# Performance work log

Measured on AMD Instinct MI355X. Metric: run time of the kernel, lower is better.

## Reference

```python
import jax, jax.numpy as jnp
import numpy as np

H = 8  # num_heads
NEG = -1e6  # mask fill value used by the torch masked_softmax


def layernorm(x, g, b, eps=1e-5):
    mu = jnp.mean(x, axis=-1, keepdims=True)
    var = jnp.mean(jnp.square(x - mu), axis=-1, keepdims=True)
    return (x - mu) * jax.lax.rsqrt(var + eps) * g + b


def setup_inputs() -> dict:
    key = jax.random.key(0)
    ks = jax.random.split(key, 10)
    B, S, D, F = 8, 1024, 512, 2048
    s = 0.02
    return {
        "X": jax.random.normal(ks[0], (B, S, D), jnp.float32),
        "valid_lens": jax.random.randint(ks[1], (B,), 1, S + 1, jnp.int32),
        "ln1_g": jnp.ones((D,), jnp.float32),
        "ln1_b": jnp.zeros((D,), jnp.float32),
        "Wq": jax.random.normal(ks[2], (D, D), jnp.float32) * s,
        "Wk": jax.random.normal(ks[3], (D, D), jnp.float32) * s,
        "Wv": jax.random.normal(ks[4], (D, D), jnp.float32) * s,
        "Wo": jax.random.normal(ks[5], (D, D), jnp.float32) * s,
        "ln2_g": jnp.ones((D,), jnp.float32),
        "ln2_b": jnp.zeros((D,), jnp.float32),
        "W1": jax.random.normal(ks[6], (D, F), jnp.float32) * s,
        "b1": jnp.zeros((F,), jnp.float32),
        "W2": jax.random.normal(ks[7], (F, D), jnp.float32) * s,
        "b2": jnp.zeros((D,), jnp.float32),
    }


def vit_block(X, valid_lens, ln1_g, ln1_b, Wq, Wk, Wv, Wo, ln2_g, ln2_b, W1, b1, W2, b2):
    B, S, D = X.shape
    dh = D // H
    h = layernorm(X, ln1_g, ln1_b)
    # project and split heads: [B, S, H, dh]
    q = (h @ Wq).reshape(B, S, H, dh)
    k = (h @ Wk).reshape(B, S, H, dh)
    v = (h @ Wv).reshape(B, S, H, dh)
    scores = jnp.einsum("bqhd,bkhd->bhqk", q, k) / jnp.sqrt(jnp.float32(dh))
    # mask keys >= valid_len[b] with -1e6 (as in masked_softmax)
    mask = jnp.arange(S)[None, None, None, :] < valid_lens[:, None, None, None]
    scores = jnp.where(mask, scores, NEG)
    attn = jax.nn.softmax(scores, axis=-1)
    out = jnp.einsum("bhqk,bkhd->bqhd", attn, v).reshape(B, S, D)
    X = X + out @ Wo
    h2 = layernorm(X, ln2_g, ln2_b)
    mlp = jax.nn.gelu(h2 @ W1 + b1, approximate=False) @ W2 + b2
    return X + mlp


def reference(X, valid_lens, ln1_g, ln1_b, Wq, Wk, Wv, Wo, ln2_g, ln2_b, W1, b1, W2, b2):
    return vit_block(X, valid_lens, ln1_g, ln1_b, Wq, Wk, Wv, Wo, ln2_g, ln2_b, W1, b1, W2, b2)
```

## Files before the change

### kernel.cpp

```cpp
#include <hip/hip_runtime.h>
#include <math.h>

#define BB 8
#define SS 1024
#define DD 512
#define FF 2048
#define NH 8
#define MM (BB * SS)
#define LDQKV 1536

using bf8 = __attribute__((ext_vector_type(8))) short;
using f4  = __attribute__((ext_vector_type(4))) float;

#define AS1 __attribute__((address_space(1)))
#define AS3 __attribute__((address_space(3)))

__device__ __forceinline__ void gload16(const void* g, void* l) {
  __builtin_amdgcn_global_load_lds((AS1 const void*)g, (AS3 void*)l, 16, 0, 0);
}

template <int N> __device__ __forceinline__ void wait_vm() {
  if constexpr (N == 0)      asm volatile("s_waitcnt vmcnt(0)" ::: "memory");
  else if constexpr (N == 3) asm volatile("s_waitcnt vmcnt(3)" ::: "memory");
  else if constexpr (N == 4) asm volatile("s_waitcnt vmcnt(4)" ::: "memory");
  else if constexpr (N == 8) asm volatile("s_waitcnt vmcnt(8)" ::: "memory");
  else                       asm volatile("s_waitcnt vmcnt(16)" ::: "memory");
  __builtin_amdgcn_sched_barrier(0);
}

__device__ __forceinline__ void bar() {
  __builtin_amdgcn_sched_barrier(0);
  __builtin_amdgcn_s_barrier();
  __builtin_amdgcn_sched_barrier(0);
}

__device__ __forceinline__ void lgk0() {
  asm volatile("s_waitcnt lgkmcnt(0)" ::: "memory");
  __builtin_amdgcn_sched_barrier(0);
}

__device__ __forceinline__ unsigned short f2b(float f) {
  union { float f; unsigned u; } v; v.f = f;
  unsigned r = v.u + 0x7fffu + ((v.u >> 16) & 1u);
  return (unsigned short)(r >> 16);
}

__device__ __forceinline__ float gelu_f(float x) {
  float ax = fabsf(x) * 0.70710678118654752f;
  float t = 1.0f / (1.0f + 0.3275911f * ax);
  float poly = t * (0.254829592f +
               t * (-0.284496736f +
               t * (1.421413741f +
               t * (-1.453152027f + t * 1.061405429f))));
  float erfv = 1.0f - poly * __expf(-ax * ax);
  erfv = copysignf(erfv, x);
  return 0.5f * x * (1.0f + erfv);
}

__global__ __launch_bounds__(256) void ln_bf16(const float* __restrict__ x,
                                               const float* __restrict__ g,
                                               const float* __restrict__ bta,
                                               unsigned short* __restrict__ out) {
  int wave = threadIdx.x >> 6, lane = threadIdx.x & 63;
  int row = (blockIdx.x << 2) + wave;
  const float* xr = x + (size_t)row * DD;
  int base = lane << 3;
  float4 v0 = *(const float4*)(xr + base);
  float4 v1 = *(const float4*)(xr + base + 4);
  float s  = v0.x + v0.y + v0.z + v0.w + v1.x + v1.y + v1.z + v1.w;
  float sq = v0.x*v0.x + v0.y*v0.y + v0.z*v0.z + v0.w*v0.w
           + v1.x*v1.x + v1.y*v1.y + v1.z*v1.z + v1.w*v1.w;
  for (int m = 32; m; m >>= 1) { s += __shfl_xor(s, m); sq += __shfl_xor(sq, m); }
  float mu  = s * (1.0f / DD);
  float var = sq * (1.0f / DD) - mu * mu;
  float rs  = rsqrtf(var + 1e-5f);
  float xv[8], go[8], bo[8];
  *(float4*)(xv) = v0; *(float4*)(xv + 4) = v1;
  *(float4*)(go)     = *(const float4*)(g + base);
  *(float4*)(go + 4) = *(const float4*)(g + base + 4);
  *(float4*)(bo)     = *(const float4*)(bta + base);
  *(float4*)(bo + 4) = *(const float4*)(bta + base + 4);
  union { unsigned short u[8]; uint4 v; } ov;
#pragma unroll
  for (int i = 0; i < 8; i++) ov.u[i] = f2b((xv[i] - mu) * rs * go[i] + bo[i]);
  *(uint4*)(out + (size_t)row * DD + base) = ov.v;
}

__global__ __launch_bounds__(256) void tconv(const float* __restrict__ in,
                                             unsigned short* __restrict__ outp,
                                             int K, int N) {
  __shared__ float tile[32][33];
  int n0 = blockIdx.x << 5, k0 = blockIdx.y << 5;
  int c = threadIdx.x & 31, r = threadIdx.x >> 5;
#pragma unroll
  for (int i = 0; i < 4; i++)
    tile[r + 8 * i][c] = in[(size_t)(k0 + r + 8 * i) * N + n0 + c];
  __syncthreads();
#pragma unroll
  for (int i = 0; i < 4; i++)
    outp[(size_t)(n0 + r + 8 * i) * K + k0 + c] = f2b(tile[c][r + 8 * i]);
}

__global__ __launch_bounds__(256) void tconv4(
    const float* __restrict__ s0, const float* __restrict__ s1,
    const float* __restrict__ s2, const float* __restrict__ s3,
    unsigned short* __restrict__ d0, unsigned short* __restrict__ d1,
    unsigned short* __restrict__ d2, unsigned short* __restrict__ d3) {
  __shared__ float tile[32][33];
  const float* in; unsigned short* outp;
  switch (blockIdx.z) {
    case 0: in = s0; outp = d0; break;
    case 1: in = s1; outp = d1; break;
    case 2: in = s2; outp = d2; break;
    default: in = s3; outp = d3; break;
  }
  int n0 = blockIdx.x << 5, k0 = blockIdx.y << 5;
  int c = threadIdx.x & 31, r = threadIdx.x >> 5;
#pragma unroll
  for (int i = 0; i < 4; i++)
    tile[r + 8 * i][c] = in[(size_t)(k0 + r + 8 * i) * DD + n0 + c];
  __syncthreads();
#pragma unroll
  for (int i = 0; i < 4; i++)
    outp[(size_t)(n0 + r + 8 * i) * DD + k0 + c] = f2b(tile[c][r + 8 * i]);
}

template <int ACT>
__global__ __launch_bounds__(128, 2) void gemm_wp(
    const unsigned short* __restrict__ A,
    const unsigned short* __restrict__ Bt,
    const float* __restrict__ bias,
    unsigned short* __restrict__ Cb,
    int M, int N, int K, int gxn) {
  __shared__ unsigned short Lds[2][2][4096];
  int tid = threadIdx.x, wv = tid >> 6, lane = tid & 63;

  int bid = blockIdx.x, cpx = (int)gridDim.x >> 3;
  int swz = (bid & 7) * cpx + (bid >> 3);
  int tile = swz * 2 + wv;
  int m0 = (tile / gxn) << 6, n0 = (tile % gxn) << 6;

  int r4 = lane & 15, ksl = lane >> 4;
  int srow = lane >> 2;
  int gs = (lane & 3) ^ ((lane >> 3) & 3);

  const unsigned short* aSrc = A + (size_t)(m0 + srow) * K + gs * 8;
  const unsigned short* bSrc = Bt + (size_t)(n0 + srow) * K + gs * 8;
  char* lw = (char*)&Lds[wv][0][0];

  f4 acc[4][4];
#pragma unroll
  for (int i = 0; i < 4; i++)
#pragma unroll
    for (int j = 0; j < 4; j++) acc[i][j] = (f4){0.f, 0.f, 0.f, 0.f};

  auto STAGE = [&](int buf, int t) {
    int k0 = t << 5;
#pragma unroll
    for (int ch = 0; ch < 4; ch++) {
      gload16(aSrc + (size_t)(ch * 16) * K + k0, &Lds[wv][buf][ch * 512]);
      gload16(bSrc + (size_t)(ch * 16) * K + k0, &Lds[wv][buf][2048 + ch * 512]);
    }
  };

  auto COMPUTE = [&](int buf) {
    char* ab = lw + buf * 8192;
    bf8 af[4], bfr[4];
#pragma unroll
    for (int mi = 0; mi < 4; mi++) {
      int r = mi * 16 + r4;
      af[mi] = *(const bf8*)(ab + r * 64 + ((ksl ^ ((r >> 1) & 3)) << 4));
    }
#pragma unroll
    for (int ni = 0; ni < 4; ni++) {
      int r = ni * 16 + r4;
      bfr[ni] = *(const bf8*)(ab + 4096 + r * 64 + ((ksl ^ ((r >> 1) & 3)) << 4));
    }
    __builtin_amdgcn_s_setprio(1);
#pragma unroll
    for (int mi = 0; mi < 4; mi++)
#pragma unroll
      for (int ni = 0; ni < 4; ni++)
        acc[mi][ni] = __builtin_amdgcn_mfma_f32_16x16x32_bf16(
            af[mi], bfr[ni], acc[mi][ni], 0, 0, 0);
    __builtin_amdgcn_s_setprio(0);
  };

  int nt = K >> 5;
  STAGE(0, 0);
  STAGE(1, 1);
  for (int t = 0; t < nt; t++) {
    if (t + 1 < nt) wait_vm<8>();
    else            wait_vm<0>();
    COMPUTE(t & 1);
    if (t + 2 < nt) {
      lgk0();
      STAGE(t & 1, t + 2);
    }
  }

  int rq = ksl << 2;
  float bv[4];
#pragma unroll
  for (int ni = 0; ni < 4; ni++)
    bv[ni] = bias ? bias[n0 + ni * 16 + r4] : 0.0f;
#pragma unroll
  for (int ni = 0; ni < 4; ni++) {
    int col = n0 + ni * 16 + r4;
#pragma unroll
    for (int mi = 0; mi < 4; mi++) {
#pragma unroll
      for (int j = 0; j < 4; j++) {
        int row = m0 + mi * 16 + rq + j;
        float v = acc[mi][ni][j] + bv[ni];
        if (ACT) v = gelu_f(v);
        Cb[(size_t)row * N + col] = f2b(v);
      }
    }
  }
}

template <int BM, int BN, int ACT, int MINW>
__global__ __launch_bounds__(256, MINW) void gemm_t(
    const unsigned short* __restrict__ A,
    const unsigned short* __restrict__ Bt,
    const float* __restrict__ bias,
    const float* __restrict__ res,
    float* __restrict__ Cf,
    unsigned short* __restrict__ Cb,
    int M, int N, int K, int gx) {
  constexpr int WM = BM / 2, WN = BN / 2;
  constexpr int FM = WM / 16, FN = WN / 16;
  constexpr int NCHA = BM / 16;
  constexpr int NCH = (BM + BN) / 16;
  constexpr int L = NCH / 4;
  __shared__ unsigned short As[2][BM * 32];
  __shared__ unsigned short Bs[2][BN * 32];
  int tid = threadIdx.x, wid = tid >> 6, lane = tid & 63;

  int bid = blockIdx.x, cpx = (int)gridDim.x >> 3;
  int swz = (bid & 7) * cpx + (bid >> 3);
  int m0 = (swz / gx) * BM, n0 = (swz % gx) * BN;

  int wm = (wid >> 1) * WM, wn = (wid & 1) * WN;
  int r4 = lane & 15, ksl = lane >> 4;
  int srow = lane >> 2, gs = (lane & 3) ^ ((lane >> 3) & 3);

  f4 acc[FM][FN];
#pragma unroll
  for (int i = 0; i < FM; i++)
#pragma unroll
    for (int j = 0; j < FN; j++) acc[i][j] = (f4){0.f, 0.f, 0.f, 0.f};

  auto STAGE = [&](int buf, int t) {
    int k0 = t << 5;
#pragma unroll
    for (int i = 0; i < L; i++) {
      int c = wid * L + i;
      if (c < NCHA)
        gload16(A + (size_t)(m0 + c * 16 + srow) * K + k0 + gs * 8,
                &As[buf][c * 512]);
      else
        gload16(Bt + (size_t)(n0 + (c - NCHA) * 16 + srow) * K + k0 + gs * 8,
                &Bs[buf][(c - NCHA) * 512]);
    }
  };

  auto COMPUTE = [&](int buf) {
    bf8 af[FM], bfr[FN];
#pragma unroll
    for (int mi = 0; mi < FM; mi++) {
      int r = wm + mi * 16 + r4;
      af[mi] = *(const bf8*)((const char*)&As[buf][0] + r * 64 +
                             ((ksl ^ ((r >> 1) & 3)) << 4));
    }
#pragma unroll
    for (int ni = 0; ni < FN; ni++) {
      int r = wn + ni * 16 + r4;
      bfr[ni] = *(const bf8*)((const char*)&Bs[buf][0] + r * 64 +
                              ((ksl ^ ((r >> 1) & 3)) << 4));
    }
    __builtin_amdgcn_s_setprio(1);
#pragma unroll
    for (int mi = 0; mi < FM; mi++)
#pragma unroll
      for (int ni = 0; ni < FN; ni++)
        acc[mi][ni] = __builtin_amdgcn_mfma_f32_16x16x32_bf16(
            af[mi], bfr[ni], acc[mi][ni], 0, 0, 0);
    __builtin_amdgcn_s_setprio(0);
  };

  int nt = K >> 5;
  STAGE(0, 0);
  STAGE(1, 1);
  for (int t = 0; t < nt; t++) {
    if (t + 1 < nt) wait_vm<L>();
    else            wait_vm<0>();
    bar();
    COMPUTE(t & 1);
    bar();
    if (t + 2 < nt) STAGE(t & 1, t + 2);
  }

  int rq = ksl << 2;
  float bv[FN];
#pragma unroll
  for (int ni = 0; ni < FN; ni++)
    bv[ni] = bias ? bias[n0 + wn + ni * 16 + r4] : 0.0f;
#pragma unroll
  for (int ni = 0; ni < FN; ni++) {
    int col = n0 + wn + ni * 16 + r4;
#pragma unroll
    for (int mi = 0; mi < FM; mi++) {
#pragma unroll
      for (int j = 0; j < 4; j++) {
        int row = m0 + wm + mi * 16 + rq + j;
        float v = acc[mi][ni][j] + bv[ni];
        if (ACT) v = gelu_f(v);
        if (res) v += res[(size_t)row * N + col];
        if (Cf) Cf[(size_t)row * N + col] = v;
        else    Cb[(size_t)row * N + col] = f2b(v);
      }
    }
  }
}

__global__ __launch_bounds__(256) void attn_mfma(
    const unsigned short* __restrict__ QKV,
    const int* __restrict__ vlen,
    unsigned short* __restrict__ AO) {
  __shared__ unsigned short Qs[64 * 64];
  __shared__ unsigned short Ks[64 * 64];
  __shared__ unsigned short Vt[64 * 64];
  __shared__ unsigned short Ps[64 * 64];
  int b = blockIdx.z, h = blockIdx.y, q0 = blockIdx.x << 6;
  int tid = threadIdx.x, wid = tid >> 6, lane = tid & 63;
  int vl = vlen[b];
  int r4 = lane & 15, ksl = lane >> 4;

  int srow = lane >> 3;
  int gs = (lane & 7) ^ srow;
  {
    const unsigned short* qsrc =
        QKV + (size_t)(b * SS + q0 + wid * 16 + srow) * LDQKV + h * 64 + gs * 8;
    gload16(qsrc, Qs + wid * 1024);
    gload16(qsrc + (size_t)8 * LDQKV, Qs + wid * 1024 + 512);
  }
  const unsigned short* kbase =
      QKV + (size_t)(b * SS + wid * 16 + srow) * LDQKV + DD + h * 64 + gs * 8;
  int vp = tid & 31, vdg = (tid >> 5) << 3;
  const unsigned short* vbase =
      QKV + (size_t)(b * SS + 2 * vp) * LDQKV + 2 * DD + h * 64 + vdg;

  f4 o[4];
#pragma unroll
  for (int i = 0; i < 4; i++) o[i] = (f4){0.f, 0.f, 0.f, 0.f};
  float mrun[4], lrun[4];
#pragma unroll
  for (int j = 0; j < 4; j++) { mrun[j] = -3e38f; lrun[j] = 0.0f; }

  int ntiles = (vl + 63) >> 6;
  if (ntiles > 16) ntiles = 16;

  for (int t = 0; t < ntiles; t++) {
    int kg0 = t << 6;
    const unsigned short* ks = kbase + (size_t)kg0 * LDQKV;
    gload16(ks, Ks + wid * 1024);
    gload16(ks + (size_t)8 * LDQKV, Ks + wid * 1024 + 512);
    {
      const unsigned short* v0 = vbase + (size_t)kg0 * LDQKV;
      const unsigned short* v1 = v0 + LDQKV;
      unsigned short va[8], vb[8];
      *(uint4*)va = *(const uint4*)v0;
      *(uint4*)vb = *(const uint4*)v1;
#pragma unroll
      for (int i = 0; i < 8; i++) {
        int d = vdg + i;
        unsigned val = (unsigned)va[i] | ((unsigned)vb[i] << 16);
        int byte = (d << 7) + (((vp >> 2) ^ (d & 7)) << 4) + ((vp & 3) << 2);
        *(unsigned*)((char*)Vt + byte) = val;
      }
    }
    __syncthreads();

    f4 s[4];
#pragma unroll
    for (int i = 0; i < 4; i++) s[i] = (f4){0.f, 0.f, 0.f, 0.f};
#pragma unroll
    for (int k2 = 0; k2 < 2; k2++) {
      int slot = (k2 << 2) + ksl;
      int qr = (wid << 4) + r4;
      bf8 aq = *(const bf8*)((const char*)Qs + (qr << 7) + ((slot ^ (qr & 7)) << 4));
#pragma unroll
      for (int ni = 0; ni < 4; ni++) {
        int kr = (ni << 4) + r4;
        bf8 bk = *(const bf8*)((const char*)Ks + (kr << 7) + ((slot ^ (kr & 7)) << 4));
        s[ni] = __builtin_amdgcn_mfma_f32_16x16x32_bf16(aq, bk, s[ni], 0, 0, 0);
      }
    }

#pragma unroll
    for (int j = 0; j < 4; j++) {
      int qr = (wid << 4) + ((lane >> 4) << 2) + j;
      float sv[4], mx = -3e38f;
#pragma unroll
      for (int ni = 0; ni < 4; ni++) {
        float v = s[ni][j] * 0.125f;
        if (kg0 + (ni << 4) + r4 >= vl) v = -1e6f;
        sv[ni] = v;
        mx = fmaxf(mx, v);
      }
#pragma unroll
      for (int m2 = 1; m2 < 16; m2 <<= 1) mx = fmaxf(mx, __shfl_xor(mx, m2));
      float mnew = fmaxf(mrun[j], mx);
      float al = __expf(mrun[j] - mnew);
      float ls = 0.0f;
      unsigned short pb[4];
#pragma unroll
      for (int ni = 0; ni < 4; ni++) {
        float p = __expf(sv[ni] - mnew);
        ls += p;
        pb[ni] = f2b(p);
      }
#pragma unroll
      for (int m2 = 1; m2 < 16; m2 <<= 1) ls += __shfl_xor(ls, m2);
      lrun[j] = lrun[j] * al + ls;
      mrun[j] = mnew;
#pragma unroll
      for (int ni = 0; ni < 4; ni++) {
        int kc = (ni << 4) + r4;
        int byte = (qr << 7) + (((kc >> 3) ^ (qr & 7)) << 4) + ((kc & 7) << 1);
        *(unsigned short*)((char*)Ps + byte) = pb[ni];
        o[ni][j] *= al;
      }
    }

#pragma unroll
    for (int k2 = 0; k2 < 2; k2++) {
      int slot = (k2 << 2) + ksl;
      int qr = (wid << 4) + r4;
      bf8 ap = *(const bf8*)((const char*)Ps + (qr << 7) + ((slot ^ (qr & 7)) << 4));
#pragma unroll
      for (int ni = 0; ni < 4; ni++) {
        int dr = (ni << 4) + r4;
        bf8 bv = *(const bf8*)((const char*)Vt + (dr << 7) + ((slot ^ (dr & 7)) << 4));
        o[ni] = __builtin_amdgcn_mfma_f32_16x16x32_bf16(ap, bv, o[ni], 0, 0, 0);
      }
    }
    __syncthreads();
  }

  float inv[4];
#pragma unroll
  for (int j = 0; j < 4; j++) inv[j] = 1.0f / lrun[j];
#pragma unroll
  for (int ni = 0; ni < 4; ni++) {
#pragma unroll
    for (int j = 0; j < 4; j++) {
      int qr = (wid << 4) + ((lane >> 4) << 2) + j;
      int d = (ni << 4) + r4;
      AO[(size_t)(b * SS + q0 + qr) * DD + h * 64 + d] = f2b(o[ni][j] * inv[j]);
    }
  }
}

extern "C" void kernel_launch(void* const* d_in, const int* in_sizes, int n_in,
                              void* d_out, int out_size, void* d_ws,
                              size_t ws_size, hipStream_t stream) {
  const float* X    = (const float*)d_in[0];
  const int*   vln  = (const int*)d_in[1];
  const float* ln1g = (const float*)d_in[2];
  const float* ln1b = (const float*)d_in[3];
  const float* Wq   = (const float*)d_in[4];
  const float* Wk   = (const float*)d_in[5];
  const float* Wv   = (const float*)d_in[6];
  const float* Wo   = (const float*)d_in[7];
  const float* ln2g = (const float*)d_in[8];
  const float* ln2b = (const float*)d_in[9];
  const float* W1   = (const float*)d_in[10];
  const float* b1   = (const float*)d_in[11];
  const float* W2   = (const float*)d_in[12];
  const float* b2   = (const float*)d_in[13];
  float* out = (float*)d_out;

  unsigned short* ws = (unsigned short*)d_ws;
  unsigned short* h     = ws;
  unsigned short* QKVb  = h     + (size_t)MM * DD;
  unsigned short* AOb   = QKVb  + (size_t)MM * LDQKV;
  unsigned short* mid   = AOb   + (size_t)MM * DD;
  unsigned short* Wqkvt = mid   + (size_t)MM * FF;
  unsigned short* Wot   = Wqkvt + (size_t)3 * DD * DD;
  unsigned short* W1t   = Wot   + (size_t)DD * DD;
  unsigned short* W2t   = W1t   + (size_t)FF * DD;

  dim3 blk(256);
  dim3 blkw(128);

  tconv4<<<dim3(16, 16, 4), blk, 0, stream>>>(
      Wq, Wk, Wv, Wo, Wqkvt, Wqkvt + (size_t)DD * DD,
      Wqkvt + (size_t)2 * DD * DD, Wot);
  tconv<<<dim3(64, 16), blk, 0, stream>>>(W1, W1t, DD, FF);
  tconv<<<dim3(16, 64), blk, 0, stream>>>(W2, W2t, FF, DD);

  ln_bf16<<<dim3(MM / 4), blk, 0, stream>>>(X, ln1g, ln1b, h);
  gemm_wp<0><<<dim3((MM / 64) * (LDQKV / 64) / 2), blkw, 0, stream>>>(
      h, Wqkvt, nullptr, QKVb, MM, LDQKV, DD, LDQKV / 64);
  attn_mfma<<<dim3(SS / 64, NH, BB), blk, 0, stream>>>(QKVb, vln, AOb);
  gemm_t<128, 64, 0, 6><<<dim3((DD / 64) * (MM / 128)), blk, 0, stream>>>(
      AOb, Wot, nullptr, X, out, nullptr, MM, DD, DD, DD / 64);
  ln_bf16<<<dim3(MM / 4), blk, 0, stream>>>(out, ln2g, ln2b, h);
  gemm_wp<1><<<dim3((MM / 64) * (FF / 64) / 2), blkw, 0, stream>>>(
      h, W1t, b1, mid, MM, FF, DD, FF / 64);
  gemm_t<128, 64, 0, 6><<<dim3((DD / 64) * (MM / 128)), blk, 0, stream>>>(
      mid, W2t, b2, out, out, nullptr, MM, DD, FF, DD / 64);
}
```

Before: 201.1 us.

## Pre-pack LN output and weights into MFMA fragment layout, drop LDS staging

LayerNorm and the QKV/W1 weight conversion now write bf16 data directly in MFMA-fragment-packed order. This lets the QKV and FC1 GEMMs load operands straight from global memory into registers, with no LDS staging. The GEMM tile changes from per-wave 64x64 tiles with LDS double buffering to 128x128 blocks of four waves using register double buffering. This removes LDS traffic and waits, but each wave now reloads shared operands from global or L2 memory without LDS reuse, and more packing kernels run.

```diff
diff --git a/kernel.cpp b/kernel.cpp
--- a/kernel.cpp
+++ b/kernel.cpp
@@ -31,11 +31,6 @@
 __device__ __forceinline__ void bar() {
   __builtin_amdgcn_sched_barrier(0);
   __builtin_amdgcn_s_barrier();
-  __builtin_amdgcn_sched_barrier(0);
-}
-
-__device__ __forceinline__ void lgk0() {
-  asm volatile("s_waitcnt lgkmcnt(0)" ::: "memory");
   __builtin_amdgcn_sched_barrier(0);
 }
 
@@ -57,33 +52,57 @@
   return 0.5f * x * (1.0f + erfv);
 }
 
-__global__ __launch_bounds__(256) void ln_bf16(const float* __restrict__ x,
-                                               const float* __restrict__ g,
-                                               const float* __restrict__ bta,
-                                               unsigned short* __restrict__ out) {
-  int wave = threadIdx.x >> 6, lane = threadIdx.x & 63;
-  int row = (blockIdx.x << 2) + wave;
-  const float* xr = x + (size_t)row * DD;
-  int base = lane << 3;
-  float4 v0 = *(const float4*)(xr + base);
-  float4 v1 = *(const float4*)(xr + base + 4);
-  float s  = v0.x + v0.y + v0.z + v0.w + v1.x + v1.y + v1.z + v1.w;
-  float sq = v0.x*v0.x + v0.y*v0.y + v0.z*v0.z + v0.w*v0.w
-           + v1.x*v1.x + v1.y*v1.y + v1.z*v1.z + v1.w*v1.w;
-  for (int m = 32; m; m >>= 1) { s += __shfl_xor(s, m); sq += __shfl_xor(sq, m); }
+
+__global__ __launch_bounds__(256) void ln_pk(const float* __restrict__ x,
+                                             const float* __restrict__ g,
+                                             const float* __restrict__ bta,
+                                             unsigned short* __restrict__ outp) {
+  int tid = threadIdx.x, w = tid >> 6, l = tid & 63;
+  int panel = blockIdx.x;
+  int rl = (w << 2) + (l >> 4);
+  int r = (panel << 4) + rl;
+  int c = l & 15;
+  const float* xr = x + (size_t)r * DD;
+  float v[32], gv[32], bv[32];
+#pragma unroll
+  for (int i = 0; i < 4; i++) {
+    int k0 = c * 8 + i * 128;
+    *(float4*)(v + i * 8)      = *(const float4*)(xr + k0);
+    *(float4*)(v + i * 8 + 4)  = *(const float4*)(xr + k0 + 4);
+    *(float4*)(gv + i * 8)     = *(const float4*)(g + k0);
+    *(float4*)(gv + i * 8 + 4) = *(const float4*)(g + k0 + 4);
+    *(float4*)(bv + i * 8)     = *(const float4*)(bta + k0);
+    *(float4*)(bv + i * 8 + 4) = *(const float4*)(bta + k0 + 4);
+  }
+  float s = 0.f, sq = 0.f;
+#pragma unroll
+  for (int i = 0; i < 32; i++) { s += v[i]; sq += v[i] * v[i]; }
+  for (int m = 1; m < 16; m <<= 1) { s += __shfl_xor(s, m); sq += __shfl_xor(sq, m); }
   float mu  = s * (1.0f / DD);
   float var = sq * (1.0f / DD) - mu * mu;
   float rs  = rsqrtf(var + 1e-5f);
-  float xv[8], go[8], bo[8];
-  *(float4*)(xv) = v0; *(float4*)(xv + 4) = v1;
-  *(float4*)(go)     = *(const float4*)(g + base);
-  *(float4*)(go + 4) = *(const float4*)(g + base + 4);
-  *(float4*)(bo)     = *(const float4*)(bta + base);
-  *(float4*)(bo + 4) = *(const float4*)(bta + base + 4);
-  union { unsigned short u[8]; uint4 v; } ov;
-#pragma unroll
-  for (int i = 0; i < 8; i++) ov.u[i] = f2b((xv[i] - mu) * rs * go[i] + bo[i]);
-  *(uint4*)(out + (size_t)row * DD + base) = ov.v;
+#pragma unroll
+  for (int i = 0; i < 4; i++) {
+    int kblk = (c >> 2) + i * 4;
+    int lane_f = rl | ((c & 3) << 4);
+    union { unsigned short u[8]; uint4 q; } o;
+#pragma unroll
+    for (int j = 0; j < 8; j++)
+      o.u[j] = f2b((v[i * 8 + j] - mu) * rs * gv[i * 8 + j] + bv[i * 8 + j]);
+    *(uint4*)(outp + ((size_t)panel * 16 + kblk) * 512 + lane_f * 8) = o.q;
+  }
+}
+
+__global__ __launch_bounds__(64) void pack_w(const float* __restrict__ W,
+                                             unsigned short* __restrict__ outp,
+                                             int K, int N) {
+  int np = blockIdx.x, kb = blockIdx.y, l = threadIdx.x;
+  int n = np * 16 + (l & 15);
+  int k0 = kb * 32 + (l >> 4) * 8;
+  union { unsigned short u[8]; uint4 q; } o;
+#pragma unroll
+  for (int i = 0; i < 8; i++) o.u[i] = f2b(W[(size_t)(k0 + i) * N + n]);
+  *(uint4*)(outp + ((size_t)np * (K >> 5) + kb) * 512 + l * 8) = o.q;
 }
 
 __global__ __launch_bounds__(256) void tconv(const float* __restrict__ in,
@@ -101,52 +120,27 @@
     outp[(size_t)(n0 + r + 8 * i) * K + k0 + c] = f2b(tile[c][r + 8 * i]);
 }
 
-__global__ __launch_bounds__(256) void tconv4(
-    const float* __restrict__ s0, const float* __restrict__ s1,
-    const float* __restrict__ s2, const float* __restrict__ s3,
-    unsigned short* __restrict__ d0, unsigned short* __restrict__ d1,
-    unsigned short* __restrict__ d2, unsigned short* __restrict__ d3) {
-  __shared__ float tile[32][33];
-  const float* in; unsigned short* outp;
-  switch (blockIdx.z) {
-    case 0: in = s0; outp = d0; break;
-    case 1: in = s1; outp = d1; break;
-    case 2: in = s2; outp = d2; break;
-    default: in = s3; outp = d3; break;
-  }
-  int n0 = blockIdx.x << 5, k0 = blockIdx.y << 5;
-  int c = threadIdx.x & 31, r = threadIdx.x >> 5;
-#pragma unroll
-  for (int i = 0; i < 4; i++)
-    tile[r + 8 * i][c] = in[(size_t)(k0 + r + 8 * i) * DD + n0 + c];
-  __syncthreads();
-#pragma unroll
-  for (int i = 0; i < 4; i++)
-    outp[(size_t)(n0 + r + 8 * i) * DD + k0 + c] = f2b(tile[c][r + 8 * i]);
-}
-
-template <int ACT>
-__global__ __launch_bounds__(128, 2) void gemm_wp(
-    const unsigned short* __restrict__ A,
-    const unsigned short* __restrict__ Bt,
+template <int NT, int ACT>
+__global__ __launch_bounds__(256) void gemm_pk(
+    const unsigned short* __restrict__ pkA,
+    const unsigned short* __restrict__ pkB,
     const float* __restrict__ bias,
     unsigned short* __restrict__ Cb,
-    int M, int N, int K, int gxn) {
-  __shared__ unsigned short Lds[2][2][4096];
-  int tid = threadIdx.x, wv = tid >> 6, lane = tid & 63;
-
+    int M, int N, int gx) {
+  int tid = threadIdx.x, wid = tid >> 6, lane = tid & 63;
   int bid = blockIdx.x, cpx = (int)gridDim.x >> 3;
   int swz = (bid & 7) * cpx + (bid >> 3);
-  int tile = swz * 2 + wv;
-  int m0 = (tile / gxn) << 6, n0 = (tile % gxn) << 6;
-
+  int m0 = (swz / gx) << 7, n0 = (swz % gx) << 7;
+  int wm = (wid >> 1) << 6, wn = (wid & 1) << 6;
   int r4 = lane & 15, ksl = lane >> 4;
-  int srow = lane >> 2;
-  int gs = (lane & 3) ^ ((lane >> 3) & 3);
-
-  const unsigned short* aSrc = A + (size_t)(m0 + srow) * K + gs * 8;
-  const unsigned short* bSrc = Bt + (size_t)(n0 + srow) * K + gs * 8;
-  char* lw = (char*)&Lds[wv][0][0];
+
+  const unsigned short* aP[4];
+  const unsigned short* bP[4];
+#pragma unroll
+  for (int i = 0; i < 4; i++) {
+    aP[i] = pkA + ((size_t)(((m0 + wm) >> 4) + i) * NT) * 512 + lane * 8;
+    bP[i] = pkB + ((size_t)(((n0 + wn) >> 4) + i) * NT) * 512 + lane * 8;
+  }
 
   f4 acc[4][4];
 #pragma unroll
@@ -154,64 +148,48 @@
 #pragma unroll
     for (int j = 0; j < 4; j++) acc[i][j] = (f4){0.f, 0.f, 0.f, 0.f};
 
-  auto STAGE = [&](int buf, int t) {
-    int k0 = t << 5;
-#pragma unroll
-    for (int ch = 0; ch < 4; ch++) {
-      gload16(aSrc + (size_t)(ch * 16) * K + k0, &Lds[wv][buf][ch * 512]);
-      gload16(bSrc + (size_t)(ch * 16) * K + k0, &Lds[wv][buf][2048 + ch * 512]);
+  bf8 ca[4], cb[4], na[4], nb[4];
+
+  auto LOADS = [&](bf8 (&da)[4], bf8 (&db)[4], int t) {
+#pragma unroll
+    for (int i = 0; i < 4; i++) {
+      da[i] = *(const bf8*)(aP[i] + t * 512);
+      db[i] = *(const bf8*)(bP[i] + t * 512);
     }
   };
-
-  auto COMPUTE = [&](int buf) {
-    char* ab = lw + buf * 8192;
-    bf8 af[4], bfr[4];
-#pragma unroll
-    for (int mi = 0; mi < 4; mi++) {
-      int r = mi * 16 + r4;
-      af[mi] = *(const bf8*)(ab + r * 64 + ((ksl ^ ((r >> 1) & 3)) << 4));
-    }
-#pragma unroll
-    for (int ni = 0; ni < 4; ni++) {
-      int r = ni * 16 + r4;
-      bfr[ni] = *(const bf8*)(ab + 4096 + r * 64 + ((ksl ^ ((r >> 1) & 3)) << 4));
-    }
+  auto STEP = [&](bf8 (&da)[4], bf8 (&db)[4]) {
     __builtin_amdgcn_s_setprio(1);
 #pragma unroll
     for (int mi = 0; mi < 4; mi++)
 #pragma unroll
       for (int ni = 0; ni < 4; ni++)
         acc[mi][ni] = __builtin_amdgcn_mfma_f32_16x16x32_bf16(
-            af[mi], bfr[ni], acc[mi][ni], 0, 0, 0);
+            da[mi], db[ni], acc[mi][ni], 0, 0, 0);
     __builtin_amdgcn_s_setprio(0);
   };
 
-  int nt = K >> 5;
-  STAGE(0, 0);
-  STAGE(1, 1);
-  for (int t = 0; t < nt; t++) {
-    if (t + 1 < nt) wait_vm<8>();
-    else            wait_vm<0>();
-    COMPUTE(t & 1);
-    if (t + 2 < nt) {
-      lgk0();
-      STAGE(t & 1, t + 2);
-    }
+  LOADS(ca, cb, 0);
+#pragma unroll
+  for (int t = 0; t < NT; t += 2) {
+    if (t + 1 < NT) LOADS(na, nb, t + 1);
+    STEP(ca, cb);
+    if (t + 2 < NT) LOADS(ca, cb, t + 2);
+    if (t + 1 < NT) STEP(na, nb);
   }
 
   int rq = ksl << 2;
   float bv[4];
 #pragma unroll
   for (int ni = 0; ni < 4; ni++)
-    bv[ni] = bias ? bias[n0 + ni * 16 + r4] : 0.0f;
+    bv[ni] = bias ? bias[n0 + wn + ni * 16 + r4] : 0.0f;
 #pragma unroll
   for (int ni = 0; ni < 4; ni++) {
-    int col = n0 + ni * 16 + r4;
+    int col = n0 + wn + ni * 16 + r4;
 #pragma unroll
     for (int mi = 0; mi < 4; mi++) {
 #pragma unroll
       for (int j = 0; j < 4; j++) {
-        int row = m0 + mi * 16 + rq + j;
+        int row = m0 + wm + mi * 16 + rq + j;
         float v = acc[mi][ni][j] + bv[ni];
         if (ACT) v = gelu_f(v);
         Cb[(size_t)row * N + col] = f2b(v);
@@ -484,33 +462,33 @@
   float* out = (float*)d_out;
 
   unsigned short* ws = (unsigned short*)d_ws;
-  unsigned short* h     = ws;
-  unsigned short* QKVb  = h     + (size_t)MM * DD;
+  unsigned short* hp    = ws;
+  unsigned short* QKVb  = hp    + (size_t)MM * DD;
   unsigned short* AOb   = QKVb  + (size_t)MM * LDQKV;
   unsigned short* mid   = AOb   + (size_t)MM * DD;
-  unsigned short* Wqkvt = mid   + (size_t)MM * FF;
-  unsigned short* Wot   = Wqkvt + (size_t)3 * DD * DD;
-  unsigned short* W1t   = Wot   + (size_t)DD * DD;
-  unsigned short* W2t   = W1t   + (size_t)FF * DD;
+  unsigned short* pkQKV = mid   + (size_t)MM * FF;
+  unsigned short* pkW1  = pkQKV + (size_t)3 * DD * DD;
+  unsigned short* Wot   = pkW1  + (size_t)FF * DD;
+  unsigned short* W2t   = Wot   + (size_t)DD * DD;
 
   dim3 blk(256);
-  dim3 blkw(128);
-
-  tconv4<<<dim3(16, 16, 4), blk, 0, stream>>>(
-      Wq, Wk, Wv, Wo, Wqkvt, Wqkvt + (size_t)DD * DD,
-      Wqkvt + (size_t)2 * DD * DD, Wot);
-  tconv<<<dim3(64, 16), blk, 0, stream>>>(W1, W1t, DD, FF);
+
+  pack_w<<<dim3(32, 16), dim3(64), 0, stream>>>(Wq, pkQKV, DD, DD);
+  pack_w<<<dim3(32, 16), dim3(64), 0, stream>>>(Wk, pkQKV + (size_t)DD * DD, DD, DD);
+  pack_w<<<dim3(32, 16), dim3(64), 0, stream>>>(Wv, pkQKV + (size_t)2 * DD * DD, DD, DD);
+  pack_w<<<dim3(128, 16), dim3(64), 0, stream>>>(W1, pkW1, DD, FF);
+  tconv<<<dim3(16, 16), blk, 0, stream>>>(Wo, Wot, DD, DD);
   tconv<<<dim3(16, 64), blk, 0, stream>>>(W2, W2t, FF, DD);
 
-  ln_bf16<<<dim3(MM / 4), blk, 0, stream>>>(X, ln1g, ln1b, h);
-  gemm_wp<0><<<dim3((MM / 64) * (LDQKV / 64) / 2), blkw, 0, stream>>>(
-      h, Wqkvt, nullptr, QKVb, MM, LDQKV, DD, LDQKV / 64);
+  ln_pk<<<dim3(MM / 16), blk, 0, stream>>>(X, ln1g, ln1b, hp);
+  gemm_pk<16, 0><<<dim3((MM / 128) * (LDQKV / 128)), blk, 0, stream>>>(
+      hp, pkQKV, nullptr, QKVb, MM, LDQKV, LDQKV / 128);
   attn_mfma<<<dim3(SS / 64, NH, BB), blk, 0, stream>>>(QKVb, vln, AOb);
   gemm_t<128, 64, 0, 6><<<dim3((DD / 64) * (MM / 128)), blk, 0, stream>>>(
       AOb, Wot, nullptr, X, out, nullptr, MM, DD, DD, DD / 64);
-  ln_bf16<<<dim3(MM / 4), blk, 0, stream>>>(out, ln2g, ln2b, h);
-  gemm_wp<1><<<dim3((MM / 64) * (FF / 64) / 2), blkw, 0, stream>>>(
-      h, W1t, b1, mid, MM, FF, DD, FF / 64);
+  ln_pk<<<dim3(MM / 16), blk, 0, stream>>>(out, ln2g, ln2b, hp);
+  gemm_pk<16, 1><<<dim3((MM / 128) * (FF / 128)), blk, 0, stream>>>(
+      hp, pkW1, b1, mid, MM, FF, FF / 128);
   gemm_t<128, 64, 0, 6><<<dim3((DD / 64) * (MM / 128)), blk, 0, stream>>>(
       mid, W2t, b2, out, out, nullptr, MM, DD, FF, DD / 64);
 }
```

After: 182.3 us. -9.3%, faster.
